# Kernel tuning notes

Hardware: AMD Instinct MI355X
Metric: run time of the kernel (lower is better)

## Reference

```python
import jax, jax.numpy as jnp
import numpy as np

OUT_W, OUT_L, OUT_H = 7, 7, 7   # output_size
SR = 2                          # sampling_ratio (samples per bin per axis)


def setup_inputs() -> dict:
    key = jax.random.key(0)
    k1, k2, k3, k4, k5 = jax.random.split(key, 5)
    B, C, W, L, H = 2, 128, 64, 64, 64
    N = 128
    inp = jax.random.normal(k1, (B, C, W, L, H), jnp.float32)
    bidx = jax.random.randint(k2, (N,), 0, B).astype(jnp.float32)
    ctr = jax.random.uniform(k3, (N, 3), minval=8.0, maxval=56.0)
    size = jax.random.uniform(k4, (N, 3), minval=8.0, maxval=32.0)
    theta = jax.random.uniform(k5, (N, 1), minval=-np.pi, maxval=np.pi)
    rois = jnp.concatenate([bidx[:, None], ctr, size, theta], axis=1)  # [N,8]
    return {"input": inp, "rois": rois, "spatial_scale": jnp.float32(1.0)}


def _trilinear_gather(vol, b, x, y, z):
    # vol: [B,W,L,H,C]; b: [N]; x,y,z: [N,PW,PL,PH] float coords.
    B, W, L, H, C = vol.shape
    valid = (x > -1.0) & (x < W) & (y > -1.0) & (y < L) & (z > -1.0) & (z < H)
    x = jnp.clip(x, 0.0, W - 1.0)
    y = jnp.clip(y, 0.0, L - 1.0)
    z = jnp.clip(z, 0.0, H - 1.0)
    x0 = jnp.floor(x).astype(jnp.int32)
    y0 = jnp.floor(y).astype(jnp.int32)
    z0 = jnp.floor(z).astype(jnp.int32)
    x1 = jnp.minimum(x0 + 1, W - 1)
    y1 = jnp.minimum(y0 + 1, L - 1)
    z1 = jnp.minimum(z0 + 1, H - 1)
    lx = x - x0; hx = 1.0 - lx
    ly = y - y0; hy = 1.0 - ly
    lz = z - z0; hz = 1.0 - lz
    bb = b[:, None, None, None]

    def g(xi, yi, zi):
        return vol[bb, xi, yi, zi]  # [N,PW,PL,PH,C]

    out = (g(x0, y0, z0) * (hx * hy * hz)[..., None]
           + g(x1, y0, z0) * (lx * hy * hz)[..., None]
           + g(x0, y1, z0) * (hx * ly * hz)[..., None]
           + g(x1, y1, z0) * (lx * ly * hz)[..., None]
           + g(x0, y0, z1) * (hx * hy * lz)[..., None]
           + g(x1, y0, z1) * (lx * hy * lz)[..., None]
           + g(x0, y1, z1) * (hx * ly * lz)[..., None]
           + g(x1, y1, z1) * (lx * ly * lz)[..., None])
    return out * valid[..., None]


def _axis_offsets(size, nbins):
    # size: [N]; returns [N, nbins*SR] local coords centered at 0.
    binw = size / nbins
    i = jnp.arange(nbins * SR, dtype=jnp.float32)
    return (-size * 0.5)[:, None] + (i[None, :] + 0.5) * (binw / SR)[:, None]


def roi_align_rotated_3d(input, rois, spatial_scale):
    B, C, W, L, H = input.shape
    vol = jnp.transpose(input, (0, 2, 3, 4, 1))  # [B,W,L,H,C]
    b = rois[:, 0].astype(jnp.int32)
    ctr = rois[:, 1:4] * spatial_scale           # cx,cy,cz
    size = rois[:, 4:7] * spatial_scale          # w,l,h
    theta = rois[:, 7]
    N = rois.shape[0]

    xx = _axis_offsets(size[:, 0], OUT_W)[:, :, None, None]  # [N,PW,1,1]
    yy = _axis_offsets(size[:, 1], OUT_L)[:, None, :, None]  # [N,1,PL,1]
    zz = _axis_offsets(size[:, 2], OUT_H)[:, None, None, :]  # [N,1,1,PH]

    c = jnp.cos(theta)[:, None, None, None]
    s = jnp.sin(theta)[:, None, None, None]
    # rotate sample offsets about z-axis, then shift to ROI center
    x = c * xx - s * yy + ctr[:, 0][:, None, None, None]
    y = s * xx + c * yy + ctr[:, 1][:, None, None, None]
    z = jnp.broadcast_to(zz + ctr[:, 2][:, None, None, None],
                         (N, OUT_W * SR, OUT_L * SR, OUT_H * SR))
    x = jnp.broadcast_to(x, z.shape)
    y = jnp.broadcast_to(y, z.shape)

    vals = _trilinear_gather(vol, b, x, y, z)  # [N,PW,PL,PH,C]
    vals = vals.reshape(N, OUT_W, SR, OUT_L, SR, OUT_H, SR, C)
    pooled = vals.mean(axis=(2, 4, 6))          # [N,OW,OL,OH,C]
    return jnp.transpose(pooled, (0, 4, 1, 2, 3))  # [N,C,OW,OL,OH]


def reference(input, rois, spatial_scale):
    return roi_align_rotated_3d(input, rois, spatial_scale)
```

## Files before the change

### kernel.cpp

```cpp
#include <hip/hip_runtime.h>

#define OUT_W 7
#define OUT_L 7
#define OUT_H 7
#define SR 2
#define CDIM 128
#define WDIM 64
#define LDIM 64
#define HDIM 64
#define VOLSZ (WDIM * LDIM * HDIM)
#define NSAMP (OUT_W * SR * OUT_L * SR)
#define CSTRIDE 52
#define WINF 48
#define NGROUPS 96

typedef float f4 __attribute__((ext_vector_type(4)));

#define GLOAD0(dst, p)  asm volatile("global_load_dwordx4 %0, %1, off"           : "=v"(dst) : "v"(p))
#define GLOAD16(dst, p) asm volatile("global_load_dwordx4 %0, %1, off offset:16" : "=v"(dst) : "v"(p))
#define GLOAD32(dst, p) asm volatile("global_load_dwordx4 %0, %1, off offset:32" : "=v"(dst) : "v"(p))

__global__ __launch_bounds__(384, 5) void roi_align_rot3d_kernel(
    const float* __restrict__ input, const float* __restrict__ rois,
    const float* __restrict__ scale_ptr, float* __restrict__ out, int N)
{
    __shared__ int4   colb[NSAMP];
    __shared__ float4 colw[NSAMP];
    __shared__ alignas(16) float icol[NSAMP][CSTRIDE];
    __shared__ alignas(16) float zw[OUT_H][8];
    __shared__ int zb4s[OUT_H];

    const int nwg = N * CDIM;
    const int q = nwg >> 3, rr = nwg & 7;
    const int xcd = blockIdx.x & 7;
    const int idx_in = blockIdx.x >> 3;
    const int wk = (xcd < rr ? xcd * (q + 1) : rr * (q + 1) + (xcd - rr) * q) + idx_in;
    const int c0 = wk / N;
    const int n  = wk - c0 * N;
    const int t = threadIdx.x;

    const float scale = scale_ptr[0];
    const float* r = rois + (size_t)n * 8;
    const int   b  = (int)r[0];
    const float cx = r[1] * scale, cy = r[2] * scale, cz = r[3] * scale;
    const float sx = r[4] * scale, sy = r[5] * scale, szv = r[6] * scale;
    const float th = r[7];
    const float ct = cosf(th), st = sinf(th);

    if (t < NSAMP) {
        const int isx = t / 14, isy = t - isx * 14;
        const float xx = -0.5f * sx + ((float)isx + 0.5f) * (sx * (1.0f / 14.0f));
        const float yy = -0.5f * sy + ((float)isy + 0.5f) * (sy * (1.0f / 14.0f));
        float x = ct * xx - st * yy + cx;
        float y = st * xx + ct * yy + cy;
        const bool v = (x > -1.0f) && (x < (float)WDIM) && (y > -1.0f) && (y < (float)LDIM);
        x = fminf(fmaxf(x, 0.0f), (float)(WDIM - 1));
        y = fminf(fmaxf(y, 0.0f), (float)(LDIM - 1));
        const int x0 = (int)floorf(x);
        const int y0 = (int)floorf(y);
        const int x1 = min(x0 + 1, WDIM - 1);
        const int y1 = min(y0 + 1, LDIM - 1);
        const float lx = x - (float)x0, ly = y - (float)y0;
        const float hx = 1.0f - lx, hy = 1.0f - ly;
        const float vm = v ? 1.0f : 0.0f;
        int4 cb;
        cb.x = x0 * (LDIM * HDIM) + y0 * HDIM;
        cb.y = x1 * (LDIM * HDIM) + y0 * HDIM;
        cb.z = x0 * (LDIM * HDIM) + y1 * HDIM;
        cb.w = x1 * (LDIM * HDIM) + y1 * HDIM;
        colb[t] = cb;
        float4 cw;
        cw.x = hx * hy * vm; cw.y = lx * hy * vm;
        cw.z = hx * ly * vm; cw.w = lx * ly * vm;
        colw[t] = cw;
    } else if (t < NSAMP + OUT_H) {
        const int oh = t - NSAMP;
        float w8[8];
        #pragma unroll
        for (int k = 0; k < 8; ++k) w8[k] = 0.0f;
        int zb4 = 0;
        #pragma unroll
        for (int dz = 0; dz < 2; ++dz) {
            const int s = oh * 2 + dz;
            const float zraw = -0.5f * szv + ((float)s + 0.5f) * (szv * (1.0f / 14.0f)) + cz;
            const bool v = (zraw > -1.0f) && (zraw < (float)HDIM);
            const float z = fminf(fmaxf(zraw, 0.0f), (float)(HDIM - 1));
            const int z0 = (int)floorf(z);
            const int z1 = min(z0 + 1, HDIM - 1);
            const float lz = z - (float)z0, hz = 1.0f - lz;
            const float vm = v ? 1.0f : 0.0f;
            if (dz == 0) zb4 = min(z0 & ~3, HDIM - 8);
            w8[z0 - zb4] += hz * vm;
            w8[z1 - zb4] += lz * vm;
        }
        zb4s[oh] = zb4;
        #pragma unroll
        for (int k = 0; k < 8; ++k) zw[oh][k] = w8[k];
    }
    __syncthreads();

    const int zbase = min(zb4s[0], HDIM - WINF);

    {
        const int g = t >> 2, lane4 = t & 3;
        const float* base = input + (size_t)(b * CDIM + c0) * (size_t)VOLSZ
                          + (zbase + lane4 * 12);
        for (int s0 = 0; s0 < NSAMP; s0 += NGROUPS) {
            const int s = s0 + g;
            if (s < NSAMP) {
                const int4   cb = colb[s];
                const float4 cw = colw[s];
                const float* a0 = base + cb.x;
                const float* a1 = base + cb.y;
                const float* a2 = base + cb.z;
                const float* a3 = base + cb.w;
                f4 d0, d1, d2, d3, d4, d5;
                GLOAD0(d0, a0); GLOAD16(d1, a0); GLOAD32(d2, a0);
                GLOAD0(d3, a1); GLOAD16(d4, a1); GLOAD32(d5, a1);
                asm volatile("s_waitcnt vmcnt(0)"
                    : "+v"(d0), "+v"(d1), "+v"(d2), "+v"(d3), "+v"(d4), "+v"(d5));
                f4 acc0 = cw.x * d0 + cw.y * d3;
                f4 acc1 = cw.x * d1 + cw.y * d4;
                f4 acc2 = cw.x * d2 + cw.y * d5;
                GLOAD0(d0, a2); GLOAD16(d1, a2); GLOAD32(d2, a2);
                GLOAD0(d3, a3); GLOAD16(d4, a3); GLOAD32(d5, a3);
                asm volatile("s_waitcnt vmcnt(0)"
                    : "+v"(d0), "+v"(d1), "+v"(d2), "+v"(d3), "+v"(d4), "+v"(d5));
                acc0 += cw.z * d0 + cw.w * d3;
                acc1 += cw.z * d1 + cw.w * d4;
                acc2 += cw.z * d2 + cw.w * d5;
                float* dst = &icol[s][lane4 * 12];
                *(f4*)(dst + 0) = acc0;
                *(f4*)(dst + 4) = acc1;
                *(f4*)(dst + 8) = acc2;
            }
        }
    }
    __syncthreads();

    if (t >= 343) return;
    const int ow = t / 49;
    const int rem = t - ow * 49;
    const int ol = rem / 7;
    const int oh = rem - ol * 7;

    const f4 zwa = *(const f4*)&zw[oh][0];
    const f4 zwb = *(const f4*)&zw[oh][4];
    const int off = zb4s[oh] - zbase;

    float acc = 0.0f;
    #pragma unroll
    for (int dx = 0; dx < 2; ++dx) {
        #pragma unroll
        for (int dy = 0; dy < 2; ++dy) {
            const int s = (ow * 2 + dx) * 14 + (ol * 2 + dy);
            const f4 va = *(const f4*)&icol[s][off];
            const f4 vb = *(const f4*)&icol[s][off + 4];
            acc += zwa.x*va.x + zwa.y*va.y + zwa.z*va.z + zwa.w*va.w
                 + zwb.x*vb.x + zwb.y*vb.y + zwb.z*vb.z + zwb.w*vb.w;
        }
    }
    out[((size_t)(n * CDIM + c0)) * 343 + t] = acc * 0.125f;
}

extern "C" void kernel_launch(void* const* d_in, const int* in_sizes, int n_in,
                              void* d_out, int out_size, void* d_ws, size_t ws_size,
                              hipStream_t stream) {
    const float* input = (const float*)d_in[0];
    const float* rois  = (const float*)d_in[1];
    const float* scale = (const float*)d_in[2];
    float* out = (float*)d_out;
    const int N = in_sizes[1] / 8;
    dim3 grid((unsigned)(N * CDIM));
    dim3 block(384);
    hipLaunchKernelGGL(roi_align_rot3d_kernel, grid, block, 0, stream,
                       input, rois, scale, out, N);
}
```

Before: 483.5 us.

## Adapt z-window width per ROI and interleave lanes across 64-byte segments

```diff
diff --git a/kernel.cpp b/kernel.cpp
--- a/kernel.cpp
+++ b/kernel.cpp
@@ -10,17 +10,18 @@
 #define HDIM 64
 #define VOLSZ (WDIM * LDIM * HDIM)
 #define NSAMP (OUT_W * SR * OUT_L * SR)
-#define CSTRIDE 52
-#define WINF 48
-#define NGROUPS 96
+#define CSTRIDE 68
+#define BLK 512
+#define NGROUPS (BLK / 4)
 
 typedef float f4 __attribute__((ext_vector_type(4)));
 
-#define GLOAD0(dst, p)  asm volatile("global_load_dwordx4 %0, %1, off"           : "=v"(dst) : "v"(p))
-#define GLOAD16(dst, p) asm volatile("global_load_dwordx4 %0, %1, off offset:16" : "=v"(dst) : "v"(p))
-#define GLOAD32(dst, p) asm volatile("global_load_dwordx4 %0, %1, off offset:32" : "=v"(dst) : "v"(p))
-
-__global__ __launch_bounds__(384, 5) void roi_align_rot3d_kernel(
+#define GLD0(d,p) asm volatile("global_load_dwordx4 %0, %1, off"            : "=v"(d) : "v"(p))
+#define GLD1(d,p) asm volatile("global_load_dwordx4 %0, %1, off offset:64"  : "=v"(d) : "v"(p))
+#define GLD2(d,p) asm volatile("global_load_dwordx4 %0, %1, off offset:128" : "=v"(d) : "v"(p))
+#define GLD3(d,p) asm volatile("global_load_dwordx4 %0, %1, off offset:192" : "=v"(d) : "v"(p))
+
+__global__ __launch_bounds__(BLK, 4) void roi_align_rot3d_kernel(
     const float* __restrict__ input, const float* __restrict__ rois,
     const float* __restrict__ scale_ptr, float* __restrict__ out, int N)
 {
@@ -99,40 +100,70 @@
     }
     __syncthreads();
 
-    const int zbase = min(zb4s[0], HDIM - WINF);
+    const int zlo16 = zb4s[0] & ~15;
+    int nl = (zb4s[6] + 8 - zlo16 + 15) >> 4;
+    if (nl < 2) nl = 2;
+    const int zb0 = min(zlo16, HDIM - 16 * nl);
 
     {
         const int g = t >> 2, lane4 = t & 3;
-        const float* base = input + (size_t)(b * CDIM + c0) * (size_t)VOLSZ
-                          + (zbase + lane4 * 12);
-        for (int s0 = 0; s0 < NSAMP; s0 += NGROUPS) {
-            const int s = s0 + g;
+        const float* bcol = input + (size_t)(b * CDIM + c0) * (size_t)VOLSZ
+                          + zb0 + lane4 * 4;
+        #pragma unroll
+        for (int it = 0; it < 2; ++it) {
+            const int s = g + it * NGROUPS;
             if (s < NSAMP) {
                 const int4   cb = colb[s];
                 const float4 cw = colw[s];
-                const float* a0 = base + cb.x;
-                const float* a1 = base + cb.y;
-                const float* a2 = base + cb.z;
-                const float* a3 = base + cb.w;
-                f4 d0, d1, d2, d3, d4, d5;
-                GLOAD0(d0, a0); GLOAD16(d1, a0); GLOAD32(d2, a0);
-                GLOAD0(d3, a1); GLOAD16(d4, a1); GLOAD32(d5, a1);
-                asm volatile("s_waitcnt vmcnt(0)"
-                    : "+v"(d0), "+v"(d1), "+v"(d2), "+v"(d3), "+v"(d4), "+v"(d5));
-                f4 acc0 = cw.x * d0 + cw.y * d3;
-                f4 acc1 = cw.x * d1 + cw.y * d4;
-                f4 acc2 = cw.x * d2 + cw.y * d5;
-                GLOAD0(d0, a2); GLOAD16(d1, a2); GLOAD32(d2, a2);
-                GLOAD0(d3, a3); GLOAD16(d4, a3); GLOAD32(d5, a3);
-                asm volatile("s_waitcnt vmcnt(0)"
-                    : "+v"(d0), "+v"(d1), "+v"(d2), "+v"(d3), "+v"(d4), "+v"(d5));
-                acc0 += cw.z * d0 + cw.w * d3;
-                acc1 += cw.z * d1 + cw.w * d4;
-                acc2 += cw.z * d2 + cw.w * d5;
-                float* dst = &icol[s][lane4 * 12];
-                *(f4*)(dst + 0) = acc0;
-                *(f4*)(dst + 4) = acc1;
-                *(f4*)(dst + 8) = acc2;
+                const float* p0 = bcol + cb.x;
+                const float* p1 = bcol + cb.y;
+                const float* p2 = bcol + cb.z;
+                const float* p3 = bcol + cb.w;
+                float* dst = &icol[s][lane4 * 4];
+                switch (nl) {
+                case 2: {
+                    f4 d00, d01, d10, d11, d20, d21, d30, d31;
+                    GLD0(d00, p0); GLD1(d01, p0);
+                    GLD0(d10, p1); GLD1(d11, p1);
+                    GLD0(d20, p2); GLD1(d21, p2);
+                    GLD0(d30, p3); GLD1(d31, p3);
+                    asm volatile("s_waitcnt vmcnt(0)"
+                        : "+v"(d00), "+v"(d01), "+v"(d10), "+v"(d11),
+                          "+v"(d20), "+v"(d21), "+v"(d30), "+v"(d31));
+                    *(f4*)(dst +  0) = cw.x*d00 + cw.y*d10 + cw.z*d20 + cw.w*d30;
+                    *(f4*)(dst + 16) = cw.x*d01 + cw.y*d11 + cw.z*d21 + cw.w*d31;
+                } break;
+                case 3: {
+                    f4 d00, d01, d02, d10, d11, d12, d20, d21, d22, d30, d31, d32;
+                    GLD0(d00, p0); GLD1(d01, p0); GLD2(d02, p0);
+                    GLD0(d10, p1); GLD1(d11, p1); GLD2(d12, p1);
+                    GLD0(d20, p2); GLD1(d21, p2); GLD2(d22, p2);
+                    GLD0(d30, p3); GLD1(d31, p3); GLD2(d32, p3);
+                    asm volatile("s_waitcnt vmcnt(0)"
+                        : "+v"(d00), "+v"(d01), "+v"(d02), "+v"(d10), "+v"(d11), "+v"(d12),
+                          "+v"(d20), "+v"(d21), "+v"(d22), "+v"(d30), "+v"(d31), "+v"(d32));
+                    *(f4*)(dst +  0) = cw.x*d00 + cw.y*d10 + cw.z*d20 + cw.w*d30;
+                    *(f4*)(dst + 16) = cw.x*d01 + cw.y*d11 + cw.z*d21 + cw.w*d31;
+                    *(f4*)(dst + 32) = cw.x*d02 + cw.y*d12 + cw.z*d22 + cw.w*d32;
+                } break;
+                default: {
+                    f4 d00, d01, d02, d03, d10, d11, d12, d13;
+                    f4 d20, d21, d22, d23, d30, d31, d32, d33;
+                    GLD0(d00, p0); GLD1(d01, p0); GLD2(d02, p0); GLD3(d03, p0);
+                    GLD0(d10, p1); GLD1(d11, p1); GLD2(d12, p1); GLD3(d13, p1);
+                    GLD0(d20, p2); GLD1(d21, p2); GLD2(d22, p2); GLD3(d23, p2);
+                    GLD0(d30, p3); GLD1(d31, p3); GLD2(d32, p3); GLD3(d33, p3);
+                    asm volatile("s_waitcnt vmcnt(0)"
+                        : "+v"(d00), "+v"(d01), "+v"(d02), "+v"(d03),
+                          "+v"(d10), "+v"(d11), "+v"(d12), "+v"(d13),
+                          "+v"(d20), "+v"(d21), "+v"(d22), "+v"(d23),
+                          "+v"(d30), "+v"(d31), "+v"(d32), "+v"(d33));
+                    *(f4*)(dst +  0) = cw.x*d00 + cw.y*d10 + cw.z*d20 + cw.w*d30;
+                    *(f4*)(dst + 16) = cw.x*d01 + cw.y*d11 + cw.z*d21 + cw.w*d31;
+                    *(f4*)(dst + 32) = cw.x*d02 + cw.y*d12 + cw.z*d22 + cw.w*d32;
+                    *(f4*)(dst + 48) = cw.x*d03 + cw.y*d13 + cw.z*d23 + cw.w*d33;
+                } break;
+                }
             }
         }
     }
@@ -146,7 +177,7 @@
 
     const f4 zwa = *(const f4*)&zw[oh][0];
     const f4 zwb = *(const f4*)&zw[oh][4];
-    const int off = zb4s[oh] - zbase;
+    const int off = zb4s[oh] - zb0;
 
     float acc = 0.0f;
     #pragma unroll
@@ -172,7 +203,7 @@
     float* out = (float*)d_out;
     const int N = in_sizes[1] / 8;
     dim3 grid((unsigned)(N * CDIM));
-    dim3 block(384);
+    dim3 block(BLK);
     hipLaunchKernelGGL(roi_align_rot3d_kernel, grid, block, 0, stream,
                        input, rois, scale, out, N);
 }
```

New measurement: 450.9 us. 6.7% less time.
